# Optimization experiments

Hardware: AMD Instinct MI355X
Metric: run time of the kernel (lower is better)

## Reference

```python
import jax, jax.numpy as jnp
import numpy as np

N, E = 50000, 800000
D_IN, D_H, D_OUT = 128, 256, 128
EPS = 1e-5  # BatchNorm eps


def _glorot(key, fan_in, fan_out):
    s = jnp.sqrt(6.0 / (fan_in + fan_out))
    return jax.random.uniform(key, (fan_in, fan_out), jnp.float32, -s, s)


def setup_inputs() -> dict:
    key = jax.random.key(0)
    ks = jax.random.split(key, 8)
    x = jax.random.normal(ks[0], (N, D_IN), jnp.float32)
    edge_index = jax.random.randint(ks[1], (2, E), 0, N, dtype=jnp.int64)
    return {
        "x": x,
        "edge_index": edge_index,
        # GCNConv layer 0: input_dim -> hidden
        "W0": _glorot(ks[2], D_IN, D_H), "b0": jnp.zeros((D_H,), jnp.float32),
        "g0": jnp.ones((D_H,), jnp.float32), "be0": jnp.zeros((D_H,), jnp.float32),
        # GCNConv layer 1: hidden -> hidden (residual middle layer)
        "W1": _glorot(ks[3], D_H, D_H), "b1": jnp.zeros((D_H,), jnp.float32),
        "g1": jnp.ones((D_H,), jnp.float32), "be1": jnp.zeros((D_H,), jnp.float32),
        # GCNConv layer 2: hidden -> output
        "W2": _glorot(ks[4], D_H, D_OUT), "b2": jnp.zeros((D_OUT,), jnp.float32),
    }


def reference(x, edge_index, W0, b0, g0, be0, W1, b1, g1, be1, W2, b2):
    n = x.shape[0]
    loop = jnp.arange(n, dtype=edge_index.dtype)
    src = jnp.concatenate([edge_index[0], loop])  # add self loops
    dst = jnp.concatenate([edge_index[1], loop])
    # symmetric GCN normalization: deg computed over destinations (self loops weight 1)
    deg = jax.ops.segment_sum(jnp.ones_like(src, x.dtype), dst, num_segments=n)
    dinv = jnp.where(deg > 0, jax.lax.rsqrt(deg), 0.0)
    norm = dinv[src] * dinv[dst]  # [E+N]

    def conv(h, W, b):
        m = h @ W                              # [N, F_out] transform first (F_out small)
        m = m[src] * norm[:, None]             # gather + edge scale
        return jax.ops.segment_sum(m, dst, num_segments=n) + b

    def bn(h, g, be):  # training-mode batch stats over the node dim
        mu = h.mean(axis=0)
        var = h.var(axis=0)
        return (h - mu) * jax.lax.rsqrt(var + EPS) * g + be

    # layer 0
    h = jax.nn.relu(bn(conv(x, W0, b0), g0, be0))
    # middle residual layer
    h = jax.nn.relu(bn(conv(h, W1, b1), g1, be1)) + h
    # output layer + input residual (input_dim == output_dim, no projection)
    h = conv(h, W2, b2)
    return h + x
```

## Files before the change

### kernel.cpp

```cpp
#include <hip/hip_runtime.h>

#define BN_EPS 1e-5f

static constexpr int D_IN = 128;

using u16 = unsigned short;
using f32x4  = __attribute__((ext_vector_type(4))) float;
using bf16x8 = __attribute__((ext_vector_type(8))) __bf16;

union FragU { uint4 u; bf16x8 v; };

__device__ __forceinline__ u16 f2bf(float f) {
  unsigned int u = __float_as_uint(f);
  u += 0x7FFFu + ((u >> 16) & 1u);
  return (u16)(u >> 16);
}
__device__ __forceinline__ float bf2f(u16 h) {
  return __uint_as_float(((unsigned int)h) << 16);
}


__global__ __launch_bounds__(256) void zero_kernel(int* __restrict__ p, int n) {
  int i = blockIdx.x * 256 + threadIdx.x;
  if (i < n) p[i] = 0;
}

__global__ __launch_bounds__(256) void count_kernel(const int* __restrict__ dst, int E,
                                                    int* __restrict__ cnt) {
  int e = blockIdx.x * 256 + threadIdx.x;
  if (e < E) atomicAdd(&cnt[dst[e]], 1);
}

__global__ __launch_bounds__(1024) void scan_sum_kernel(const int* __restrict__ cnt, int n,
                                                        int* __restrict__ bsum,
                                                        float* __restrict__ dinv) {
  __shared__ int sdata[1024];
  int i = blockIdx.x * 1024 + threadIdx.x;
  int v = (i < n) ? cnt[i] : 0;
  if (i < n) dinv[i] = rsqrtf((float)v + 1.0f);
  sdata[threadIdx.x] = v;
  __syncthreads();
  for (int s = 512; s > 0; s >>= 1) {
    if (threadIdx.x < s) sdata[threadIdx.x] += sdata[threadIdx.x + s];
    __syncthreads();
  }
  if (threadIdx.x == 0) bsum[blockIdx.x] = sdata[0];
}

__global__ void scan_off_kernel(const int* __restrict__ bsum, int nb,
                                int* __restrict__ boff, int* __restrict__ rowptr_last) {
  if (threadIdx.x == 0 && blockIdx.x == 0) {
    int run = 0;
    for (int b = 0; b < nb; ++b) { boff[b] = run; run += bsum[b]; }
    *rowptr_last = run;
  }
}

__global__ __launch_bounds__(1024) void scan_final_kernel(const int* __restrict__ cnt, int n,
                                                          const int* __restrict__ boff,
                                                          int* __restrict__ rowptr) {
  __shared__ int wt[16];
  int i = blockIdx.x * 1024 + threadIdx.x;
  int lane = threadIdx.x & 63, w = threadIdx.x >> 6;
  int v = (i < n) ? cnt[i] : 0;
  int x = v;
  #pragma unroll
  for (int d = 1; d < 64; d <<= 1) {
    int t = __shfl_up(x, d, 64);
    if (lane >= d) x += t;
  }
  if (lane == 63) wt[w] = x;
  __syncthreads();
  if (threadIdx.x == 0) {
    int run = 0;
    #pragma unroll
    for (int k = 0; k < 16; ++k) { int t = wt[k]; wt[k] = run; run += t; }
  }
  __syncthreads();
  if (i < n) rowptr[i] = x - v + wt[w] + boff[blockIdx.x];
}

__global__ __launch_bounds__(256) void fill_kernel(const int* __restrict__ src,
                                                   const int* __restrict__ dst, int E,
                                                   const int* __restrict__ rowptr,
                                                   int* __restrict__ cursor, int* __restrict__ col) {
  int e = blockIdx.x * 256 + threadIdx.x;
  if (e < E) {
    int d = dst[e];
    int p = atomicAdd(&cursor[d], 1);
    col[rowptr[d] + p] = src[e];
  }
}


__global__ __launch_bounds__(256) void prep_kernel(const float* __restrict__ x, u16* __restrict__ x_bf,
                                                   const float* __restrict__ W0, u16* __restrict__ Wt0,
                                                   const float* __restrict__ W1, u16* __restrict__ Wt1,
                                                   const float* __restrict__ W2, u16* __restrict__ Wt2,
                                                   int N, int BX) {
  int b = blockIdx.x, tid = threadIdx.x;
  if (b < BX) {
    int i = b * 256 + tid;
    if (i < N * 32) {
      float4 v = ((const float4*)x)[i];
      u16 o[4] = { f2bf(v.x), f2bf(v.y), f2bf(v.z), f2bf(v.w) };
      ((uint2*)x_bf)[i] = *(uint2*)o;
    }
  } else if (b < BX + 128) {
    int idx = (b - BX) * 256 + tid;
    int k = idx >> 8, nc = idx & 255;
    Wt0[nc * 128 + k] = f2bf(W0[idx]);
  } else if (b < BX + 384) {
    int idx = (b - BX - 128) * 256 + tid;
    int k = idx >> 8, nc = idx & 255;
    Wt1[nc * 256 + k] = f2bf(W1[idx]);
  } else {
    int idx = (b - BX - 384) * 256 + tid;
    int k = idx >> 7, nc = idx & 127;
    Wt2[nc * 256 + k] = f2bf(W2[idx]);
  }
}


template<int F, bool BIAS, bool FINAL>
__global__ __launch_bounds__(256) void agg_bf16(const u16* __restrict__ in,
                                                const int* __restrict__ rowptr,
                                                const int* __restrict__ col,
                                                const float* __restrict__ dinv,
                                                const float* __restrict__ bias,
                                                const float* __restrict__ xres,
                                                void* __restrict__ outv, int n) {
  constexpr int V = F / 64;
  int node = blockIdx.x * 4 + (threadIdx.x >> 6);
  if (node >= n) return;
  int lane = threadIdx.x & 63;
  const int off = lane * V;
  const size_t rowbase = (size_t)node * F + off;

  float di = dinv[node];
  float acc[V];
  {
    u16 t[V];
    if constexpr (V == 4) *(uint2*)t = *(const uint2*)(in + rowbase);
    else                  *(unsigned int*)t = *(const unsigned int*)(in + rowbase);
    #pragma unroll
    for (int j = 0; j < V; ++j) acc[j] = di * bf2f(t[j]);
  }

  int e   = __builtin_amdgcn_readfirstlane(rowptr[node]);
  int end = __builtin_amdgcn_readfirstlane(rowptr[node + 1]);
  for (; e + 4 <= end; e += 4) {
    int s0 = col[e], s1 = col[e + 1], s2 = col[e + 2], s3 = col[e + 3];
    float w0 = dinv[s0], w1 = dinv[s1], w2 = dinv[s2], w3 = dinv[s3];
    u16 t0[V], t1[V], t2[V], t3[V];
    if constexpr (V == 4) {
      *(uint2*)t0 = *(const uint2*)(in + (size_t)s0 * F + off);
      *(uint2*)t1 = *(const uint2*)(in + (size_t)s1 * F + off);
      *(uint2*)t2 = *(const uint2*)(in + (size_t)s2 * F + off);
      *(uint2*)t3 = *(const uint2*)(in + (size_t)s3 * F + off);
    } else {
      *(unsigned int*)t0 = *(const unsigned int*)(in + (size_t)s0 * F + off);
      *(unsigned int*)t1 = *(const unsigned int*)(in + (size_t)s1 * F + off);
      *(unsigned int*)t2 = *(const unsigned int*)(in + (size_t)s2 * F + off);
      *(unsigned int*)t3 = *(const unsigned int*)(in + (size_t)s3 * F + off);
    }
    #pragma unroll
    for (int j = 0; j < V; ++j) acc[j] = fmaf(w0, bf2f(t0[j]), acc[j]);
    #pragma unroll
    for (int j = 0; j < V; ++j) acc[j] = fmaf(w1, bf2f(t1[j]), acc[j]);
    #pragma unroll
    for (int j = 0; j < V; ++j) acc[j] = fmaf(w2, bf2f(t2[j]), acc[j]);
    #pragma unroll
    for (int j = 0; j < V; ++j) acc[j] = fmaf(w3, bf2f(t3[j]), acc[j]);
  }
  for (; e < end; ++e) {
    int s0 = col[e];
    float w0 = dinv[s0];
    u16 t0[V];
    if constexpr (V == 4) *(uint2*)t0 = *(const uint2*)(in + (size_t)s0 * F + off);
    else                  *(unsigned int*)t0 = *(const unsigned int*)(in + (size_t)s0 * F + off);
    #pragma unroll
    for (int j = 0; j < V; ++j) acc[j] = fmaf(w0, bf2f(t0[j]), acc[j]);
  }

  #pragma unroll
  for (int j = 0; j < V; ++j) acc[j] *= di;
  if constexpr (BIAS) {
    #pragma unroll
    for (int j = 0; j < V; ++j) acc[j] += bias[off + j];
  }
  if constexpr (FINAL) {
    float* out = (float*)outv;
    float xr[V];
    if constexpr (V == 2) *(float2*)xr = *(const float2*)(xres + rowbase);
    else                  *(float4*)xr = *(const float4*)(xres + rowbase);
    #pragma unroll
    for (int j = 0; j < V; ++j) acc[j] += xr[j];
    if constexpr (V == 2) *(float2*)(out + rowbase) = *(float2*)acc;
    else                  *(float4*)(out + rowbase) = *(float4*)acc;
  } else {
    u16* out = (u16*)outv;
    u16 o[V];
    #pragma unroll
    for (int j = 0; j < V; ++j) o[j] = f2bf(acc[j]);
    if constexpr (V == 4) *(uint2*)(out + rowbase) = *(uint2*)o;
    else                  *(unsigned int*)(out + rowbase) = *(unsigned int*)o;
  }
}


template<int K, int NN, bool BIAS, bool STATS>
__global__ __launch_bounds__(256) void gemm_bf16(const u16* __restrict__ A,
                                                 const u16* __restrict__ Wt,
                                                 const float* __restrict__ bias,
                                                 u16* __restrict__ C,
                                                 float* __restrict__ partial, int M) {
  __shared__ u16 As[2][128 * 64];
  __shared__ u16 Bs[2][128 * 64];
  __shared__ float sstat[256];
  const int tid = threadIdx.x;
  const int lane = tid & 63;
  const int wid = tid >> 6;
  const int wm = wid >> 1, wn = wid & 1;
  const int bm = blockIdx.x * 128;
  const int bn = blockIdx.y * 128;
  const int srow = tid >> 3;
  const int schunk = tid & 7;

  if constexpr (STATS) sstat[tid] = 0.f;

  f32x4 acc[4][4] = {};

  auto stage = [&](int buf, int k0) {
    #pragma unroll
    for (int p = 0; p < 4; ++p) {
      int r = srow + p * 32;
      int rg = bm + r; if (rg >= M) rg = M - 1;
      int sc = schunk ^ (r & 7);
      __builtin_amdgcn_global_load_lds(
          (const __attribute__((address_space(1))) void*)(A + (size_t)rg * K + k0 + sc * 8),
          (__attribute__((address_space(3))) void*)(&As[buf][r * 64 + schunk * 8]),
          16, 0, 0);
    }
    #pragma unroll
    for (int p = 0; p < 4; ++p) {
      int r = srow + p * 32;
      int sc = schunk ^ (r & 7);
      __builtin_amdgcn_global_load_lds(
          (const __attribute__((address_space(1))) void*)(Wt + (size_t)(bn + r) * K + k0 + sc * 8),
          (__attribute__((address_space(3))) void*)(&Bs[buf][r * 64 + schunk * 8]),
          16, 0, 0);
    }
  };

  stage(0, 0);
  __syncthreads();

  constexpr int NT = K / 64;
  int buf = 0;
  #pragma unroll
  for (int t = 0; t < NT; ++t) {
    if (t + 1 < NT) stage(buf ^ 1, (t + 1) * 64);
    #pragma unroll
    for (int ks = 0; ks < 2; ++ks) {
      FragU a[4], b[4];
      #pragma unroll
      for (int mt = 0; mt < 4; ++mt) {
        int r = wm * 64 + mt * 16 + (lane & 15);
        int c = ks * 4 + (lane >> 4);
        a[mt].u = *(const uint4*)(&As[buf][r * 64 + ((c ^ (r & 7)) * 8)]);
      }
      #pragma unroll
      for (int nt = 0; nt < 4; ++nt) {
        int r = wn * 64 + nt * 16 + (lane & 15);
        int c = ks * 4 + (lane >> 4);
        b[nt].u = *(const uint4*)(&Bs[buf][r * 64 + ((c ^ (r & 7)) * 8)]);
      }
      #pragma unroll
      for (int mt = 0; mt < 4; ++mt)
        #pragma unroll
        for (int nt = 0; nt < 4; ++nt)
          acc[mt][nt] = __builtin_amdgcn_mfma_f32_16x16x32_bf16(a[mt].v, b[nt].v,
                                                                acc[mt][nt], 0, 0, 0);
    }
    __syncthreads();
    buf ^= 1;
  }

  #pragma unroll
  for (int nt = 0; nt < 4; ++nt) {
    int cl = wn * 64 + nt * 16 + (lane & 15);
    int gc = bn + cl;
    float bv = 0.f;
    if constexpr (BIAS) bv = bias[gc];
    float cs = 0.f, cq = 0.f;
    #pragma unroll
    for (int mt = 0; mt < 4; ++mt) {
      int gr0 = bm + wm * 64 + mt * 16 + (lane >> 4) * 4;
      #pragma unroll
      for (int j = 0; j < 4; ++j) {
        int gr = gr0 + j;
        if (gr < M) {
          float v = acc[mt][nt][j] + bv;
          C[(size_t)gr * NN + gc] = f2bf(v);
          if constexpr (STATS) { cs += v; cq = fmaf(v, v, cq); }
        }
      }
    }
    if constexpr (STATS) {
      cs += __shfl_xor(cs, 16, 64); cq += __shfl_xor(cq, 16, 64);
      cs += __shfl_xor(cs, 32, 64); cq += __shfl_xor(cq, 32, 64);
      if ((lane >> 4) == 0) {
        atomicAdd(&sstat[cl], cs);
        atomicAdd(&sstat[128 + cl], cq);
      }
    }
  }
  if constexpr (STATS) {
    __syncthreads();
    if (tid < 128) {
      size_t pb = ((size_t)blockIdx.y * gridDim.x + blockIdx.x) * 256;
      partial[pb + tid]       = sstat[tid];
      partial[pb + 128 + tid] = sstat[128 + tid];
    }
  }
}


__global__ __launch_bounds__(64) void finalize_gemm(const float* __restrict__ partial, int GX, int n,
                                                    const float* __restrict__ g,
                                                    const float* __restrict__ be,
                                                    float* __restrict__ scale,
                                                    float* __restrict__ shift) {
  int c = blockIdx.x;
  int by = c >> 7, cl = c & 127;
  float s = 0.f, q = 0.f;
  for (int bx = threadIdx.x; bx < GX; bx += 64) {
    const float* pb = partial + ((size_t)by * GX + bx) * 256;
    s += pb[cl]; q += pb[128 + cl];
  }
  #pragma unroll
  for (int d = 32; d > 0; d >>= 1) { s += __shfl_down(s, d, 64); q += __shfl_down(q, d, 64); }
  if (threadIdx.x == 0) {
    float inv_n = 1.0f / (float)n;
    float mu = s * inv_n;
    float var = q * inv_n - mu * mu;
    float rs = rsqrtf(var + BN_EPS);
    float sc = rs * g[c];
    scale[c] = sc;
    shift[c] = fmaf(-mu, sc, be[c]);
  }
}

template<int F>
__global__ __launch_bounds__(256) void stats_bf16(const u16* __restrict__ m, int n,
                                                  float* __restrict__ partial) {
  constexpr int COLS = F / 4;
  constexpr int RG = 256 / COLS;
  int c4 = threadIdx.x % COLS;
  int rg = threadIdx.x / COLS;
  float s[4] = {}, q[4] = {};
  for (int r = blockIdx.x * RG + rg; r < n; r += gridDim.x * RG) {
    u16 t[4];
    *(uint2*)t = *(const uint2*)(m + (size_t)r * F + c4 * 4);
    #pragma unroll
    for (int j = 0; j < 4; ++j) { float v = bf2f(t[j]); s[j] += v; q[j] = fmaf(v, v, q[j]); }
  }
  __shared__ float ls[256][8];
  #pragma unroll
  for (int j = 0; j < 4; ++j) { ls[threadIdx.x][j] = s[j]; ls[threadIdx.x][4 + j] = q[j]; }
  __syncthreads();
  if (rg == 0) {
    for (int g = 1; g < RG; ++g) {
      #pragma unroll
      for (int j = 0; j < 4; ++j) {
        s[j] += ls[g * COLS + c4][j];
        q[j] += ls[g * COLS + c4][4 + j];
      }
    }
    #pragma unroll
    for (int j = 0; j < 4; ++j) {
      partial[(size_t)blockIdx.x * 2 * F + c4 * 4 + j]     = s[j];
      partial[(size_t)blockIdx.x * 2 * F + F + c4 * 4 + j] = q[j];
    }
  }
}

template<int F>
__global__ __launch_bounds__(64) void finalize_agg(const float* __restrict__ partial, int nb, int n,
                                                   const float* __restrict__ g,
                                                   const float* __restrict__ be,
                                                   float* __restrict__ scale,
                                                   float* __restrict__ shift) {
  int c = blockIdx.x;
  float s = 0.f, q = 0.f;
  for (int b = threadIdx.x; b < nb; b += 64) {
    s += partial[(size_t)b * 2 * F + c];
    q += partial[(size_t)b * 2 * F + F + c];
  }
  #pragma unroll
  for (int d = 32; d > 0; d >>= 1) { s += __shfl_down(s, d, 64); q += __shfl_down(q, d, 64); }
  if (threadIdx.x == 0) {
    float inv_n = 1.0f / (float)n;
    float mu = s * inv_n;
    float var = q * inv_n - mu * mu;
    float rs = rsqrtf(var + BN_EPS);
    float sc = rs * g[c];
    scale[c] = sc;
    shift[c] = fmaf(-mu, sc, be[c]);
  }
}

template<int F, bool RES>
__global__ __launch_bounds__(256) void apply_bf16(const u16* __restrict__ m,
                                                  const float* __restrict__ scale,
                                                  const float* __restrict__ shift,
                                                  const u16* __restrict__ res,
                                                  u16* __restrict__ out, int n) {
  int i = blockIdx.x * 256 + threadIdx.x;
  if (i >= n * (F / 8)) return;
  int c = i & (F / 8 - 1);
  u16 t[8];
  *(uint4*)t = *(const uint4*)(m + (size_t)i * 8);
  float sc[8], sh[8];
  *(float4*)sc       = ((const float4*)scale)[c * 2];
  *(float4*)(sc + 4) = ((const float4*)scale)[c * 2 + 1];
  *(float4*)sh       = ((const float4*)shift)[c * 2];
  *(float4*)(sh + 4) = ((const float4*)shift)[c * 2 + 1];
  float h[8];
  #pragma unroll
  for (int j = 0; j < 8; ++j) h[j] = fmaxf(fmaf(bf2f(t[j]), sc[j], sh[j]), 0.f);
  if constexpr (RES) {
    u16 r[8];
    *(uint4*)r = *(const uint4*)(res + (size_t)i * 8);
    #pragma unroll
    for (int j = 0; j < 8; ++j) h[j] += bf2f(r[j]);
  }
  u16 o[8];
  #pragma unroll
  for (int j = 0; j < 8; ++j) o[j] = f2bf(h[j]);
  *(uint4*)(out + (size_t)i * 8) = *(uint4*)o;
}


extern "C" void kernel_launch(void* const* d_in, const int* in_sizes, int n_in,
                              void* d_out, int out_size, void* d_ws, size_t ws_size,
                              hipStream_t stream) {
  const float* x   = (const float*)d_in[0];
  const int*   ei  = (const int*)d_in[1];
  const float* W0  = (const float*)d_in[2];
  const float* b0  = (const float*)d_in[3];
  const float* g0  = (const float*)d_in[4];
  const float* be0 = (const float*)d_in[5];
  const float* W1  = (const float*)d_in[6];
  const float* b1  = (const float*)d_in[7];
  const float* g1  = (const float*)d_in[8];
  const float* be1 = (const float*)d_in[9];
  const float* W2  = (const float*)d_in[10];
  const float* b2  = (const float*)d_in[11];
  float* out = (float*)d_out;

  const int N = in_sizes[0] / D_IN;
  const int E = in_sizes[1] / 2;
  const int* esrc = ei;
  const int* edst = ei + E;

  char* p = (char*)d_ws;
  auto alloc = [&](size_t bytes) { char* r = p; p += (bytes + 255) & ~(size_t)255; return r; };
  int* cnt     = (int*)alloc((size_t)2 * N * 4);
  int* cursor  = cnt + N;
  int* rowptr  = (int*)alloc(((size_t)N + 1) * 4);
  int* col     = (int*)alloc((size_t)E * 4);
  float* dinv  = (float*)alloc((size_t)N * 4);
  const int nb = (N + 1023) / 1024;
  int* bsum    = (int*)alloc((size_t)nb * 4);
  int* boff    = (int*)alloc((size_t)nb * 4);
  const int MB = (N + 127) / 128;
  constexpr int SB = 128;
  float* partial = (float*)alloc((size_t)MB * 2 * 256 * 4);
  float* scalev  = (float*)alloc(256 * 4);
  float* shiftv  = (float*)alloc(256 * 4);
  u16* Wt0 = (u16*)alloc((size_t)256 * 128 * 2);
  u16* Wt1 = (u16*)alloc((size_t)256 * 256 * 2);
  u16* Wt2 = (u16*)alloc((size_t)128 * 256 * 2);
  u16* slotX  = (u16*)alloc((size_t)N * 128 * 2);
  u16* slotAM = (u16*)alloc((size_t)N * 256 * 2);
  u16* slotMH = (u16*)alloc((size_t)N * 256 * 2);
  u16* slotAH = (u16*)alloc((size_t)N * 256 * 2);
  u16* x_bf = slotX;  u16* m2 = slotX;
  u16* a0   = slotAM; u16* m1 = slotAM;
  u16* m0   = slotMH; u16* h0 = slotMH;
  u16* a1   = slotAH; u16* h1 = slotAH;
  (void)ws_size; (void)n_in; (void)out_size;

  const int BX = (N * 32 + 255) / 256;
  zero_kernel<<<(2 * N + 255) / 256, 256, 0, stream>>>(cnt, 2 * N);
  prep_kernel<<<BX + 512, 256, 0, stream>>>(x, x_bf, W0, Wt0, W1, Wt1, W2, Wt2, N, BX);
  count_kernel<<<(E + 255) / 256, 256, 0, stream>>>(edst, E, cnt);
  scan_sum_kernel<<<nb, 1024, 0, stream>>>(cnt, N, bsum, dinv);
  scan_off_kernel<<<1, 64, 0, stream>>>(bsum, nb, boff, rowptr + N);
  scan_final_kernel<<<nb, 1024, 0, stream>>>(cnt, N, boff, rowptr);
  fill_kernel<<<(E + 255) / 256, 256, 0, stream>>>(esrc, edst, E, rowptr, cursor, col);

  const int aggGrid = (N + 3) / 4;

  agg_bf16<128, false, false><<<aggGrid, 256, 0, stream>>>(x_bf, rowptr, col, dinv,
                                                           nullptr, nullptr, a0, N);
  gemm_bf16<128, 256, true, true><<<dim3(MB, 2), 256, 0, stream>>>(a0, Wt0, b0, m0, partial, N);
  finalize_gemm<<<256, 64, 0, stream>>>(partial, MB, N, g0, be0, scalev, shiftv);
  apply_bf16<256, false><<<(N * 32 + 255) / 256, 256, 0, stream>>>(m0, scalev, shiftv,
                                                                   nullptr, h0, N);

  gemm_bf16<256, 256, false, false><<<dim3(MB, 2), 256, 0, stream>>>(h0, Wt1, nullptr, m1,
                                                                     nullptr, N);
  agg_bf16<256, true, false><<<aggGrid, 256, 0, stream>>>(m1, rowptr, col, dinv,
                                                          b1, nullptr, a1, N);
  stats_bf16<256><<<SB, 256, 0, stream>>>(a1, N, partial);
  finalize_agg<256><<<256, 64, 0, stream>>>(partial, SB, N, g1, be1, scalev, shiftv);
  apply_bf16<256, true><<<(N * 32 + 255) / 256, 256, 0, stream>>>(a1, scalev, shiftv,
                                                                  h0, h1, N);

  gemm_bf16<256, 128, false, false><<<dim3(MB, 1), 256, 0, stream>>>(h1, Wt2, nullptr, m2,
                                                                     nullptr, N);
  agg_bf16<128, true, true><<<aggGrid, 256, 0, stream>>>(m2, rowptr, col, dinv,
                                                         b2, x, out, N);
}
```

Before: 439.5 us.

## Stream GEMMs with resident weight tile, fuse BN stats into aggregation, merge zeroing

Replaces the tiled double-buffered GEMM with a persistent kernel that loads the whole 128-column weight slice into LDS once. Each wave then streams 64-row chunks of A straight from global memory into MFMA fragments. The middle-layer aggregation now also accumulates per-column sum and sum-of-squares, which removes the separate stats pass over the activations. The zeroing kernel is folded into the prep kernel as extra blocks. The trade-offs are large LDS use per block (up to 64KB for K=256), A reads from global with no LDS reuse, and a fixed grid of 196.

```diff
diff --git a/kernel.cpp b/kernel.cpp
--- a/kernel.cpp
+++ b/kernel.cpp
@@ -19,11 +19,6 @@
   return __uint_as_float(((unsigned int)h) << 16);
 }
 
-
-__global__ __launch_bounds__(256) void zero_kernel(int* __restrict__ p, int n) {
-  int i = blockIdx.x * 256 + threadIdx.x;
-  if (i < n) p[i] = 0;
-}
 
 __global__ __launch_bounds__(256) void count_kernel(const int* __restrict__ dst, int E,
                                                     int* __restrict__ cnt) {
@@ -93,29 +88,33 @@
 }
 
 
-__global__ __launch_bounds__(256) void prep_kernel(const float* __restrict__ x, u16* __restrict__ x_bf,
+__global__ __launch_bounds__(256) void prep_kernel(int* __restrict__ zbuf, int nz, int BZ,
+                                                   const float* __restrict__ x, u16* __restrict__ x_bf,
                                                    const float* __restrict__ W0, u16* __restrict__ Wt0,
                                                    const float* __restrict__ W1, u16* __restrict__ Wt1,
                                                    const float* __restrict__ W2, u16* __restrict__ Wt2,
                                                    int N, int BX) {
   int b = blockIdx.x, tid = threadIdx.x;
-  if (b < BX) {
+  if (b < BZ) {
     int i = b * 256 + tid;
+    if (i < nz) zbuf[i] = 0;
+  } else if (b < BZ + BX) {
+    int i = (b - BZ) * 256 + tid;
     if (i < N * 32) {
       float4 v = ((const float4*)x)[i];
       u16 o[4] = { f2bf(v.x), f2bf(v.y), f2bf(v.z), f2bf(v.w) };
       ((uint2*)x_bf)[i] = *(uint2*)o;
     }
-  } else if (b < BX + 128) {
-    int idx = (b - BX) * 256 + tid;
+  } else if (b < BZ + BX + 128) {
+    int idx = (b - BZ - BX) * 256 + tid;
     int k = idx >> 8, nc = idx & 255;
     Wt0[nc * 128 + k] = f2bf(W0[idx]);
-  } else if (b < BX + 384) {
-    int idx = (b - BX - 128) * 256 + tid;
+  } else if (b < BZ + BX + 384) {
+    int idx = (b - BZ - BX - 128) * 256 + tid;
     int k = idx >> 8, nc = idx & 255;
     Wt1[nc * 256 + k] = f2bf(W1[idx]);
   } else {
-    int idx = (b - BX - 384) * 256 + tid;
+    int idx = (b - BZ - BX - 384) * 256 + tid;
     int k = idx >> 7, nc = idx & 127;
     Wt2[nc * 256 + k] = f2bf(W2[idx]);
   }
@@ -208,115 +207,176 @@
   }
 }
 
+__global__ __launch_bounds__(256) void agg_stats_bf16(const u16* __restrict__ in,
+                                                      const int* __restrict__ rowptr,
+                                                      const int* __restrict__ col,
+                                                      const float* __restrict__ dinv,
+                                                      const float* __restrict__ bias,
+                                                      u16* __restrict__ out,
+                                                      float* __restrict__ partial, int n) {
+  constexpr int F = 256, V = 4;
+  __shared__ float sstat[512];
+  const int tid = threadIdx.x;
+  const int lane = tid & 63, wid = tid >> 6;
+  const int off = lane * V;
+  sstat[tid] = 0.f; sstat[tid + 256] = 0.f;
+  __syncthreads();
+
+  float s[V] = {}, q[V] = {};
+  int base = blockIdx.x * 32 + wid * 8;
+  for (int i = 0; i < 8; ++i) {
+    int node = base + i;
+    if (node >= n) break;
+    const size_t rowbase = (size_t)node * F + off;
+    float di = dinv[node];
+    float acc[V];
+    {
+      u16 t[V];
+      *(uint2*)t = *(const uint2*)(in + rowbase);
+      #pragma unroll
+      for (int j = 0; j < V; ++j) acc[j] = di * bf2f(t[j]);
+    }
+    int e   = __builtin_amdgcn_readfirstlane(rowptr[node]);
+    int end = __builtin_amdgcn_readfirstlane(rowptr[node + 1]);
+    for (; e + 4 <= end; e += 4) {
+      int s0 = col[e], s1 = col[e + 1], s2 = col[e + 2], s3 = col[e + 3];
+      float w0 = dinv[s0], w1 = dinv[s1], w2 = dinv[s2], w3 = dinv[s3];
+      u16 t0[V], t1[V], t2[V], t3[V];
+      *(uint2*)t0 = *(const uint2*)(in + (size_t)s0 * F + off);
+      *(uint2*)t1 = *(const uint2*)(in + (size_t)s1 * F + off);
+      *(uint2*)t2 = *(const uint2*)(in + (size_t)s2 * F + off);
+      *(uint2*)t3 = *(const uint2*)(in + (size_t)s3 * F + off);
+      #pragma unroll
+      for (int j = 0; j < V; ++j) acc[j] = fmaf(w0, bf2f(t0[j]), acc[j]);
+      #pragma unroll
+      for (int j = 0; j < V; ++j) acc[j] = fmaf(w1, bf2f(t1[j]), acc[j]);
+      #pragma unroll
+      for (int j = 0; j < V; ++j) acc[j] = fmaf(w2, bf2f(t2[j]), acc[j]);
+      #pragma unroll
+      for (int j = 0; j < V; ++j) acc[j] = fmaf(w3, bf2f(t3[j]), acc[j]);
+    }
+    for (; e < end; ++e) {
+      int s0 = col[e];
+      float w0 = dinv[s0];
+      u16 t0[V];
+      *(uint2*)t0 = *(const uint2*)(in + (size_t)s0 * F + off);
+      #pragma unroll
+      for (int j = 0; j < V; ++j) acc[j] = fmaf(w0, bf2f(t0[j]), acc[j]);
+    }
+    u16 o[V];
+    #pragma unroll
+    for (int j = 0; j < V; ++j) {
+      acc[j] = fmaf(acc[j], di, bias[off + j]);
+      s[j] += acc[j]; q[j] = fmaf(acc[j], acc[j], q[j]);
+      o[j] = f2bf(acc[j]);
+    }
+    *(uint2*)(out + rowbase) = *(uint2*)o;
+  }
+  #pragma unroll
+  for (int j = 0; j < V; ++j) atomicAdd(&sstat[off + j], s[j]);
+  #pragma unroll
+  for (int j = 0; j < V; ++j) atomicAdd(&sstat[256 + off + j], q[j]);
+  __syncthreads();
+  float* pb = partial + (size_t)blockIdx.x * 512;
+  pb[tid] = sstat[tid];
+  pb[tid + 256] = sstat[tid + 256];
+}
+
 
 template<int K, int NN, bool BIAS, bool STATS>
-__global__ __launch_bounds__(256) void gemm_bf16(const u16* __restrict__ A,
-                                                 const u16* __restrict__ Wt,
-                                                 const float* __restrict__ bias,
-                                                 u16* __restrict__ C,
-                                                 float* __restrict__ partial, int M) {
-  __shared__ u16 As[2][128 * 64];
-  __shared__ u16 Bs[2][128 * 64];
+__global__ __launch_bounds__(256, 2) void gemm_stream(const u16* __restrict__ A,
+                                                      const u16* __restrict__ Wt,
+                                                      const float* __restrict__ bias,
+                                                      u16* __restrict__ C,
+                                                      float* __restrict__ partial, int M) {
+  constexpr int CPR = K / 8;
+  __shared__ u16 Blds[128 * K];
   __shared__ float sstat[256];
   const int tid = threadIdx.x;
   const int lane = tid & 63;
   const int wid = tid >> 6;
-  const int wm = wid >> 1, wn = wid & 1;
-  const int bm = blockIdx.x * 128;
   const int bn = blockIdx.y * 128;
-  const int srow = tid >> 3;
-  const int schunk = tid & 7;
-
-  if constexpr (STATS) sstat[tid] = 0.f;
-
-  f32x4 acc[4][4] = {};
-
-  auto stage = [&](int buf, int k0) {
-    #pragma unroll
-    for (int p = 0; p < 4; ++p) {
-      int r = srow + p * 32;
-      int rg = bm + r; if (rg >= M) rg = M - 1;
-      int sc = schunk ^ (r & 7);
-      __builtin_amdgcn_global_load_lds(
-          (const __attribute__((address_space(1))) void*)(A + (size_t)rg * K + k0 + sc * 8),
-          (__attribute__((address_space(3))) void*)(&As[buf][r * 64 + schunk * 8]),
-          16, 0, 0);
-    }
-    #pragma unroll
-    for (int p = 0; p < 4; ++p) {
-      int r = srow + p * 32;
-      int sc = schunk ^ (r & 7);
-      __builtin_amdgcn_global_load_lds(
-          (const __attribute__((address_space(1))) void*)(Wt + (size_t)(bn + r) * K + k0 + sc * 8),
-          (__attribute__((address_space(3))) void*)(&Bs[buf][r * 64 + schunk * 8]),
-          16, 0, 0);
-    }
-  };
-
-  stage(0, 0);
+  const int kh = lane >> 4;
+
+  if constexpr (STATS) { sstat[tid] = 0.f; }
+
+  const u16* Bsrc = Wt + (size_t)bn * K;
+  #pragma unroll
+  for (int i = 0; i < CPR / 2; ++i) {
+    int flat = i * 256 + tid;
+    int r = flat / CPR;
+    int c = flat & (CPR - 1);
+    __builtin_amdgcn_global_load_lds(
+        (const __attribute__((address_space(1))) void*)(Bsrc + (size_t)r * K + (c ^ (r & 7)) * 8),
+        (__attribute__((address_space(3))) void*)(&Blds[flat * 8]),
+        16, 0, 0);
+  }
   __syncthreads();
 
-  constexpr int NT = K / 64;
-  int buf = 0;
-  #pragma unroll
-  for (int t = 0; t < NT; ++t) {
-    if (t + 1 < NT) stage(buf ^ 1, (t + 1) * 64);
-    #pragma unroll
-    for (int ks = 0; ks < 2; ++ks) {
-      FragU a[4], b[4];
-      #pragma unroll
-      for (int mt = 0; mt < 4; ++mt) {
-        int r = wm * 64 + mt * 16 + (lane & 15);
-        int c = ks * 4 + (lane >> 4);
-        a[mt].u = *(const uint4*)(&As[buf][r * 64 + ((c ^ (r & 7)) * 8)]);
+  float cs[8] = {}, cq[8] = {};
+  const int nch = (M + 63) / 64;
+  for (int ch = blockIdx.x * 4 + wid; ch < nch; ch += gridDim.x * 4) {
+    const int r0 = ch * 64;
+    const u16* arow[4];
+    #pragma unroll
+    for (int rf = 0; rf < 4; ++rf) {
+      int row = r0 + rf * 16 + (lane & 15);
+      if (row >= M) row = M - 1;
+      arow[rf] = A + (size_t)row * K + kh * 8;
+    }
+    f32x4 acc[4][8] = {};
+    #pragma unroll
+    for (int ks = 0; ks < K / 32; ++ks) {
+      FragU a[4], b[8];
+      #pragma unroll
+      for (int rf = 0; rf < 4; ++rf)
+        a[rf].u = *(const uint4*)(arow[rf] + ks * 32);
+      #pragma unroll
+      for (int cf = 0; cf < 8; ++cf) {
+        int rr = cf * 16 + (lane & 15);
+        int c = ks * 4 + kh;
+        b[cf].u = *(const uint4*)(&Blds[rr * K + ((c ^ (rr & 7)) * 8)]);
       }
       #pragma unroll
-      for (int nt = 0; nt < 4; ++nt) {
-        int r = wn * 64 + nt * 16 + (lane & 15);
-        int c = ks * 4 + (lane >> 4);
-        b[nt].u = *(const uint4*)(&Bs[buf][r * 64 + ((c ^ (r & 7)) * 8)]);
-      }
-      #pragma unroll
-      for (int mt = 0; mt < 4; ++mt)
+      for (int rf = 0; rf < 4; ++rf)
         #pragma unroll
-        for (int nt = 0; nt < 4; ++nt)
-          acc[mt][nt] = __builtin_amdgcn_mfma_f32_16x16x32_bf16(a[mt].v, b[nt].v,
-                                                                acc[mt][nt], 0, 0, 0);
-    }
-    __syncthreads();
-    buf ^= 1;
-  }
-
-  #pragma unroll
-  for (int nt = 0; nt < 4; ++nt) {
-    int cl = wn * 64 + nt * 16 + (lane & 15);
-    int gc = bn + cl;
-    float bv = 0.f;
-    if constexpr (BIAS) bv = bias[gc];
-    float cs = 0.f, cq = 0.f;
-    #pragma unroll
-    for (int mt = 0; mt < 4; ++mt) {
-      int gr0 = bm + wm * 64 + mt * 16 + (lane >> 4) * 4;
-      #pragma unroll
-      for (int j = 0; j < 4; ++j) {
-        int gr = gr0 + j;
-        if (gr < M) {
-          float v = acc[mt][nt][j] + bv;
-          C[(size_t)gr * NN + gc] = f2bf(v);
-          if constexpr (STATS) { cs += v; cq = fmaf(v, v, cq); }
+        for (int cf = 0; cf < 8; ++cf)
+          acc[rf][cf] = __builtin_amdgcn_mfma_f32_16x16x32_bf16(a[rf].v, b[cf].v,
+                                                                acc[rf][cf], 0, 0, 0);
+    }
+    #pragma unroll
+    for (int cf = 0; cf < 8; ++cf) {
+      int gc = bn + cf * 16 + (lane & 15);
+      float bv = 0.f;
+      if constexpr (BIAS) bv = bias[gc];
+      #pragma unroll
+      for (int rf = 0; rf < 4; ++rf) {
+        int gr0 = r0 + rf * 16 + kh * 4;
+        #pragma unroll
+        for (int j = 0; j < 4; ++j) {
+          int gr = gr0 + j;
+          if (gr < M) {
+            float v = acc[rf][cf][j] + bv;
+            C[(size_t)gr * NN + gc] = f2bf(v);
+            if constexpr (STATS) { cs[cf] += v; cq[cf] = fmaf(v, v, cq[cf]); }
+          }
         }
       }
     }
-    if constexpr (STATS) {
-      cs += __shfl_xor(cs, 16, 64); cq += __shfl_xor(cq, 16, 64);
-      cs += __shfl_xor(cs, 32, 64); cq += __shfl_xor(cq, 32, 64);
-      if ((lane >> 4) == 0) {
-        atomicAdd(&sstat[cl], cs);
-        atomicAdd(&sstat[128 + cl], cq);
+  }
+
+  if constexpr (STATS) {
+    #pragma unroll
+    for (int cf = 0; cf < 8; ++cf) {
+      float s = cs[cf], q = cq[cf];
+      s += __shfl_xor(s, 16, 64); q += __shfl_xor(q, 16, 64);
+      s += __shfl_xor(s, 32, 64); q += __shfl_xor(q, 32, 64);
+      if (kh == 0) {
+        int cl = cf * 16 + (lane & 15);
+        atomicAdd(&sstat[cl], s);
+        atomicAdd(&sstat[128 + cl], q);
       }
     }
-  }
-  if constexpr (STATS) {
     __syncthreads();
     if (tid < 128) {
       size_t pb = ((size_t)blockIdx.y * gridDim.x + blockIdx.x) * 256;
@@ -352,41 +412,6 @@
   }
 }
 
-template<int F>
-__global__ __launch_bounds__(256) void stats_bf16(const u16* __restrict__ m, int n,
-                                                  float* __restrict__ partial) {
-  constexpr int COLS = F / 4;
-  constexpr int RG = 256 / COLS;
-  int c4 = threadIdx.x % COLS;
-  int rg = threadIdx.x / COLS;
-  float s[4] = {}, q[4] = {};
-  for (int r = blockIdx.x * RG + rg; r < n; r += gridDim.x * RG) {
-    u16 t[4];
-    *(uint2*)t = *(const uint2*)(m + (size_t)r * F + c4 * 4);
-    #pragma unroll
-    for (int j = 0; j < 4; ++j) { float v = bf2f(t[j]); s[j] += v; q[j] = fmaf(v, v, q[j]); }
-  }
-  __shared__ float ls[256][8];
-  #pragma unroll
-  for (int j = 0; j < 4; ++j) { ls[threadIdx.x][j] = s[j]; ls[threadIdx.x][4 + j] = q[j]; }
-  __syncthreads();
-  if (rg == 0) {
-    for (int g = 1; g < RG; ++g) {
-      #pragma unroll
-      for (int j = 0; j < 4; ++j) {
-        s[j] += ls[g * COLS + c4][j];
-        q[j] += ls[g * COLS + c4][4 + j];
-      }
-    }
-    #pragma unroll
-    for (int j = 0; j < 4; ++j) {
-      partial[(size_t)blockIdx.x * 2 * F + c4 * 4 + j]     = s[j];
-      partial[(size_t)blockIdx.x * 2 * F + F + c4 * 4 + j] = q[j];
-    }
-  }
-}
-
-template<int F>
 __global__ __launch_bounds__(64) void finalize_agg(const float* __restrict__ partial, int nb, int n,
                                                    const float* __restrict__ g,
                                                    const float* __restrict__ be,
@@ -395,8 +420,8 @@
   int c = blockIdx.x;
   float s = 0.f, q = 0.f;
   for (int b = threadIdx.x; b < nb; b += 64) {
-    s += partial[(size_t)b * 2 * F + c];
-    q += partial[(size_t)b * 2 * F + F + c];
+    s += partial[(size_t)b * 512 + c];
+    q += partial[(size_t)b * 512 + 256 + c];
   }
   #pragma unroll
   for (int d = 32; d > 0; d >>= 1) { s += __shfl_down(s, d, 64); q += __shfl_down(q, d, 64); }
@@ -475,9 +500,8 @@
   const int nb = (N + 1023) / 1024;
   int* bsum    = (int*)alloc((size_t)nb * 4);
   int* boff    = (int*)alloc((size_t)nb * 4);
-  const int MB = (N + 127) / 128;
-  constexpr int SB = 128;
-  float* partial = (float*)alloc((size_t)MB * 2 * 256 * 4);
+  const int AB = (N + 31) / 32;
+  float* partial = (float*)alloc((size_t)AB * 512 * 4);
   float* scalev  = (float*)alloc(256 * 4);
   float* shiftv  = (float*)alloc(256 * 4);
   u16* Wt0 = (u16*)alloc((size_t)256 * 128 * 2);
@@ -493,9 +517,10 @@
   u16* a1   = slotAH; u16* h1 = slotAH;
   (void)ws_size; (void)n_in; (void)out_size;
 
+  const int BZ = (2 * N + 255) / 256;
   const int BX = (N * 32 + 255) / 256;
-  zero_kernel<<<(2 * N + 255) / 256, 256, 0, stream>>>(cnt, 2 * N);
-  prep_kernel<<<BX + 512, 256, 0, stream>>>(x, x_bf, W0, Wt0, W1, Wt1, W2, Wt2, N, BX);
+  prep_kernel<<<BZ + BX + 512, 256, 0, stream>>>(cnt, 2 * N, BZ, x, x_bf,
+                                                 W0, Wt0, W1, Wt1, W2, Wt2, N, BX);
   count_kernel<<<(E + 255) / 256, 256, 0, stream>>>(edst, E, cnt);
   scan_sum_kernel<<<nb, 1024, 0, stream>>>(cnt, N, bsum, dinv);
   scan_off_kernel<<<1, 64, 0, stream>>>(bsum, nb, boff, rowptr + N);
@@ -503,25 +528,24 @@
   fill_kernel<<<(E + 255) / 256, 256, 0, stream>>>(esrc, edst, E, rowptr, cursor, col);
 
   const int aggGrid = (N + 3) / 4;
+  const int GX = 196;
 
   agg_bf16<128, false, false><<<aggGrid, 256, 0, stream>>>(x_bf, rowptr, col, dinv,
                                                            nullptr, nullptr, a0, N);
-  gemm_bf16<128, 256, true, true><<<dim3(MB, 2), 256, 0, stream>>>(a0, Wt0, b0, m0, partial, N);
-  finalize_gemm<<<256, 64, 0, stream>>>(partial, MB, N, g0, be0, scalev, shiftv);
+  gemm_stream<128, 256, true, true><<<dim3(GX, 2), 256, 0, stream>>>(a0, Wt0, b0, m0, partial, N);
+  finalize_gemm<<<256, 64, 0, stream>>>(partial, GX, N, g0, be0, scalev, shiftv);
   apply_bf16<256, false><<<(N * 32 + 255) / 256, 256, 0, stream>>>(m0, scalev, shiftv,
                                                                    nullptr, h0, N);
 
-  gemm_bf16<256, 256, false, false><<<dim3(MB, 2), 256, 0, stream>>>(h0, Wt1, nullptr, m1,
-                                                                     nullptr, N);
-  agg_bf16<256, true, false><<<aggGrid, 256, 0, stream>>>(m1, rowptr, col, dinv,
-                                                          b1, nullptr, a1, N);
-  stats_bf16<256><<<SB, 256, 0, stream>>>(a1, N, partial);
-  finalize_agg<256><<<256, 64, 0, stream>>>(partial, SB, N, g1, be1, scalev, shiftv);
+  gemm_stream<256, 256, false, false><<<dim3(GX, 2), 256, 0, stream>>>(h0, Wt1, nullptr, m1,
+                                                                       nullptr, N);
+  agg_stats_bf16<<<AB, 256, 0, stream>>>(m1, rowptr, col, dinv, b1, a1, partial, N);
+  finalize_agg<<<256, 64, 0, stream>>>(partial, AB, N, g1, be1, scalev, shiftv);
   apply_bf16<256, true><<<(N * 32 + 255) / 256, 256, 0, stream>>>(a1, scalev, shiftv,
                                                                   h0, h1, N);
 
-  gemm_bf16<256, 128, false, false><<<dim3(MB, 1), 256, 0, stream>>>(h1, Wt2, nullptr, m2,
-                                                                     nullptr, N);
+  gemm_stream<256, 128, false, false><<<dim3(GX, 1), 256, 0, stream>>>(h1, Wt2, nullptr, m2,
+                                                                       nullptr, N);
   agg_bf16<128, true, true><<<aggGrid, 256, 0, stream>>>(m2, rowptr, col, dinv,
                                                          b2, x, out, N);
 }
```

Result: faster. 409.3 us (-6.9%).
